# Kernel optimization log

Measured on AMD Instinct MI355X. Metric: run time of the kernel, lower is better.

Reference implementation:

```python
import jax, jax.numpy as jnp
import numpy as np

K = 5
PAD = K // 2
EPS = 1e-12  # F.normalize eps


def setup_inputs() -> dict:
    key = jax.random.key(0)
    k1, k2, k3 = jax.random.split(key, 3)
    b, c, h, w = 8, 1024, 64, 64
    out_ch = 1024
    feature = jax.random.normal(k1, (b, c, h, w), dtype=jnp.float32)
    # Conv2d(1024 + K*K, out_ch, 1) -> weight [out_ch, 1049], bias [out_ch]
    conv_w = jax.random.normal(k2, (out_ch, c + K * K), dtype=jnp.float32) * 0.02
    conv_b = jax.random.normal(k3, (out_ch,), dtype=jnp.float32) * 0.02
    return {"feature": feature, "conv_w": conv_w, "conv_b": conv_b}


def reference(feature, conv_w, conv_b):
    b, c, h, w = feature.shape
    # L2-normalize over channel dim (F.normalize: x / max(||x||, eps))
    norm = jnp.sqrt(jnp.sum(feature * feature, axis=1, keepdims=True))
    fn = feature / jnp.maximum(norm, EPS)
    fp = jnp.pad(fn, ((0, 0), (0, 0), (PAD, PAD), (PAD, PAD)))
    # 25 shifted correlations; order matches torch loop: index = col*K + row
    corr = jnp.stack(
        [jnp.sum(fp[:, :, r:h + r, cc:w + cc] * fn, axis=1)
         for cc in range(K) for r in range(K)],
        axis=1,
    )  # [b, K*K, h, w]
    cat = jnp.concatenate([feature, corr], axis=1)  # [b, c+K*K, h, w]
    y = jnp.einsum('oc,bchw->bohw', conv_w, cat) + conv_b[None, :, None, None]
    return jax.nn.relu(y)
```

## Files before the change

kernel.cpp:

```cpp
#include <hip/hip_runtime.h>
#include <hip/hip_bf16.h>


typedef __attribute__((ext_vector_type(8))) short short8x;
typedef __attribute__((ext_vector_type(4))) float floatx4;

#define B_   8
#define C_   1024
#define HW_  4096
#define KPAD 1088
#define NT   17

__device__ __forceinline__ unsigned short f2bf(float f) {
  unsigned int u = __float_as_uint(f);
  u += 0x7FFFu + ((u >> 16) & 1u);
  return (unsigned short)(u >> 16);
}

__device__ __forceinline__ void async16(const void* g, void* l) {
  __builtin_amdgcn_global_load_lds(
      (__attribute__((address_space(1))) void*)(void*)g,
      (__attribute__((address_space(3))) void*)l, 16, 0, 0);
}

__device__ __forceinline__ short8x rd16(const char* p) {
  return *(const short8x*)p;
}

__global__ __launch_bounds__(512) void scn_aux(
    const float* __restrict__ f, float* __restrict__ corr,
    unsigned short* __restrict__ At, const float* __restrict__ w,
    unsigned short* __restrict__ Wb) {
  __shared__ float lds2[2][64][65];
  const int n = blockIdx.x;
  const int tid = threadIdx.x;

  if (n >= 5120) {
    const int base = (n - 5120) * 4096 + tid * 8;
    const int o = base / KPAD, kk = base - o * KPAD;
    short8x v;
#pragma unroll
    for (int e = 0; e < 8; ++e) {
      const int k = kk + e;
      v[e] = (k < 1049) ? (short)f2bf(w[(size_t)o * 1049 + k]) : (short)0;
    }
    *(short8x*)(Wb + (size_t)o * KPAD + kk) = v;
    return;
  }

  const int g = n / 5, r = n - g * 5;
  if (r == 0) {
    const int x = tid & 63;
    const int y = (g & 7) * 8 + (tid >> 6);
    const int cs = (g >> 3) & 15, b = g >> 7;

    const int xs0 = (x + 2 < 64) ? x + 2 : 63;
    const int xs1 = (x + 1 < 64) ? x + 1 : 63;
    const int xs3 = (x - 1 >= 0) ? x - 1 : 0;
    const int xs4 = (x - 2 >= 0) ? x - 2 : 0;

    const bool ym2 = (y >= 2), ym1 = (y >= 1), yp1 = (y <= 62), yp2 = (y <= 61);

    const float* rp0 = f + ((size_t)b * C_ + cs * 64) * HW_ + y * 64;

    float h[25];
#pragma unroll
    for (int j = 0; j < 25; ++j) h[j] = 0.f;

#pragma unroll 4
    for (int c = 0; c < 64; ++c) {
      const float* rp = rp0 + (size_t)c * HW_;
      const float ctr = rp[x];
      const float vm2 = ym2 ? rp[x - 128] : 0.f;
      const float vm1 = ym1 ? rp[x - 64] : 0.f;
      const float vp1 = yp1 ? rp[x + 64] : 0.f;
      const float vp2 = yp2 ? rp[x + 128] : 0.f;
      const float c0 = __shfl(ctr, xs0, 64);
      const float c1 = __shfl(ctr, xs1, 64);
      const float c3 = __shfl(ctr, xs3, 64);
      const float c4 = __shfl(ctr, xs4, 64);
      const float v[5] = {vm2, vm1, ctr, vp1, vp2};
      const float cc[5] = {c0, c1, ctr, c3, c4};
#pragma unroll
      for (int dxi = 0; dxi < 5; ++dxi)
#pragma unroll
        for (int dyi = 0; dyi < 5; ++dyi)
          h[dxi * 5 + dyi] = fmaf(v[dyi], cc[dxi], h[dxi * 5 + dyi]);
    }

    float* pb = corr + b * HW_ + y * 64;
#pragma unroll
    for (int j = 0; j < 25; ++j) {
      const int dx = (j / 5) - 2;
      const int tgt = x - dx;
      const int wx = (tgt + 64) & 63;
      const float val = ((unsigned)tgt < 64u) ? h[j] : 0.f;
      atomicAdd(pb + (size_t)j * 32768 + wx, val);
    }
  } else {
    const int half = tid >> 8, t256 = tid & 255;
    const int tile = (g * 4 + (r - 1)) * 2 + half;
    const int b = tile >> 10, rem = tile & 1023;
    const int kt = rem >> 6, mt = rem & 63;

    const int m4 = (t256 & 15) << 2, kr0 = t256 >> 4;
    const float* src = f + ((size_t)b * C_ + kt * 64 + kr0) * HW_ + mt * 64 + m4;
#pragma unroll
    for (int i = 0; i < 4; ++i) {
      floatx4 v = *(const floatx4*)(src + (size_t)i * 16 * HW_);
      float* d = &lds2[half][kr0 + i * 16][m4];
      d[0] = v[0]; d[1] = v[1]; d[2] = v[2]; d[3] = v[3];
    }
    __syncthreads();
    unsigned short* dst = At + ((size_t)b * HW_ + mt * 64) * KPAD + kt * 64;
    const int c = t256 & 7, mr = t256 >> 3;
#pragma unroll
    for (int h2 = 0; h2 < 2; ++h2) {
      const int mm = mr + h2 * 32;
      short8x v;
#pragma unroll
      for (int j = 0; j < 8; ++j) v[j] = (short)f2bf(lds2[half][c * 8 + j][mm]);
      *(short8x*)(dst + (size_t)mm * KPAD + c * 8) = v;
    }
  }
}

__global__ __launch_bounds__(256) void scn_reduce2(
    const float* __restrict__ corr, unsigned short* __restrict__ At) {
  __shared__ float linv[8][64];
  const int b = blockIdx.y;
  const int bx = blockIdx.x;
  const int tid = threadIdx.x;
  const int x = tid & 63;
  const int y0 = bx * 4;

  const float* c12 = corr + (size_t)12 * 32768 + b * HW_;
#pragma unroll
  for (int rr = 0; rr < 2; ++rr) {
    const int rsel = (tid >> 6) + rr * 4;
    const int yy = y0 - 2 + rsel;
    const float s = (yy >= 0 && yy < 64) ? c12[yy * 64 + x] : 1.0f;
    linv[rsel][x] = 1.0f / fmaxf(sqrtf(s), 1e-12f);
  }
  __syncthreads();

  const int m = bx * 256 + tid;
  const int i = b * HW_ + m;
  const int yr = tid >> 6;
  const float ic = linv[yr + 2][x];

  unsigned short r[64];
#pragma unroll
  for (int j = 0; j < 25; ++j) {
    const float acc = corr[(size_t)j * 32768 + i];
    const int dy = (j % 5) - 2, dx = (j / 5) - 2;
    const int ny = y0 + yr + dy, nx = x + dx;
    const float in2 = (ny >= 0 && ny < 64 && nx >= 0 && nx < 64)
                          ? linv[yr + 2 + dy][nx] : 0.f;
    r[j] = f2bf(acc * ic * in2);
  }
#pragma unroll
  for (int j = 25; j < 64; ++j) r[j] = 0;
  unsigned short* row = At + ((size_t)b * HW_ + m) * KPAD + 1024;
#pragma unroll
  for (int v = 0; v < 8; ++v) *(short8x*)(row + v * 8) = *(short8x*)(r + v * 8);
}

__global__ __launch_bounds__(512, 2) void scn_gemm(
    const unsigned short* __restrict__ Wb, const unsigned short* __restrict__ At,
    const float* __restrict__ bias, float* __restrict__ out) {
  extern __shared__ char lds[];
  const int tid = threadIdx.x;
  const int l = tid & 63;
  const int wid = tid >> 6;
  const int wm = wid >> 2;
  const int wn = wid & 3;
  const int nb = blockIdx.x, ob = blockIdx.y, b = blockIdx.z;

  const int rr = tid >> 3;
  const int cswz = ((tid & 7) ^ (rr & 7)) << 3;
  const unsigned short* gA = Wb + (size_t)(ob * 256 + rr) * KPAD + cswz;
  const unsigned short* gB = At + ((size_t)b * HW_ + nb * 256 + rr) * KPAD + cswz;
  char* const dBase = (char*)lds + tid * 16;

#define ISSUE_A(bf, kt)                                         \
  do {                                                          \
    const unsigned short* _s = gA + (kt) * 64;                  \
    char* _d = dBase + (bf) * 65536;                            \
    async16(_s, _d);                                            \
    async16(_s + (size_t)64 * KPAD, _d + 8192);                 \
    async16(_s + (size_t)128 * KPAD, _d + 16384);               \
    async16(_s + (size_t)192 * KPAD, _d + 24576);               \
  } while (0)

#define ISSUE_B(bf, kt)                                         \
  do {                                                          \
    const unsigned short* _s = gB + (kt) * 64;                  \
    char* _d = dBase + (bf) * 65536 + 32768;                    \
    async16(_s, _d);                                            \
    async16(_s + (size_t)64 * KPAD, _d + 8192);                 \
    async16(_s + (size_t)128 * KPAD, _d + 16384);               \
    async16(_s + (size_t)192 * KPAD, _d + 24576);               \
  } while (0)

  const int l15 = l & 15, l4g = l >> 4, l7 = l & 7;
  const int aoff0 = l15 * 128 + ((l4g ^ l7) << 4);
  const int aoff1 = l15 * 128 + (((l4g + 4) ^ l7) << 4);
  const char* aB0 = (const char*)lds + wm * 16384;
  const char* bB0 = (const char*)lds + 32768 + (wn >> 1) * 16384 + (wn & 1) * 8192;

  floatx4 acc[8][4];
#pragma unroll
  for (int i = 0; i < 8; ++i)
#pragma unroll
    for (int j = 0; j < 4; ++j) acc[i][j] = (floatx4){0.f, 0.f, 0.f, 0.f};

  ISSUE_A(0, 0); ISSUE_B(0, 0);
  ISSUE_A(1, 1); ISSUE_B(1, 1);
  asm volatile("s_waitcnt vmcnt(8)" ::: "memory");
  __builtin_amdgcn_s_barrier();

  short8x a[4][2], b0[2][2], b1[2][2];

  for (int t = 0; t < NT; ++t) {
    const int bf = t & 1;
    const char* ab = aB0 + bf * 65536;
    const char* bb = bB0 + bf * 65536;
    const int t2 = (t < NT - 2) ? (t + 2) : 0;

#pragma unroll
    for (int i = 0; i < 4; ++i) {
      a[i][0] = rd16(ab + i * 2048 + aoff0);
      a[i][1] = rd16(ab + i * 2048 + aoff1);
    }
#pragma unroll
    for (int j = 0; j < 2; ++j) {
      b0[j][0] = rd16(bb + j * 2048 + aoff0);
      b0[j][1] = rd16(bb + j * 2048 + aoff1);
    }
    __builtin_amdgcn_s_barrier();
    asm volatile("s_waitcnt lgkmcnt(0)" ::: "memory");
    __builtin_amdgcn_sched_barrier(0);
    __builtin_amdgcn_s_setprio(1);
#pragma unroll
    for (int i = 0; i < 4; ++i)
#pragma unroll
      for (int j = 0; j < 2; ++j) {
        acc[i][j] = __builtin_amdgcn_mfma_f32_16x16x32_bf16(a[i][0], b0[j][0], acc[i][j], 0, 0, 0);
        acc[i][j] = __builtin_amdgcn_mfma_f32_16x16x32_bf16(a[i][1], b0[j][1], acc[i][j], 0, 0, 0);
      }
    __builtin_amdgcn_s_setprio(0);
    __builtin_amdgcn_s_barrier();

#pragma unroll
    for (int j = 0; j < 2; ++j) {
      b1[j][0] = rd16(bb + (2 + j) * 2048 + aoff0);
      b1[j][1] = rd16(bb + (2 + j) * 2048 + aoff1);
    }
    __builtin_amdgcn_s_barrier();
    asm volatile("s_waitcnt lgkmcnt(0)" ::: "memory");
    __builtin_amdgcn_sched_barrier(0);
    __builtin_amdgcn_s_setprio(1);
#pragma unroll
    for (int i = 0; i < 4; ++i)
#pragma unroll
      for (int j = 0; j < 2; ++j) {
        acc[i][2 + j] = __builtin_amdgcn_mfma_f32_16x16x32_bf16(a[i][0], b1[j][0], acc[i][2 + j], 0, 0, 0);
        acc[i][2 + j] = __builtin_amdgcn_mfma_f32_16x16x32_bf16(a[i][1], b1[j][1], acc[i][2 + j], 0, 0, 0);
      }
    __builtin_amdgcn_s_setprio(0);
    __builtin_amdgcn_s_barrier();

#pragma unroll
    for (int i = 0; i < 4; ++i) {
      a[i][0] = rd16(ab + (4 + i) * 2048 + aoff0);
      a[i][1] = rd16(ab + (4 + i) * 2048 + aoff1);
    }
    ISSUE_B(bf, t2);
    __builtin_amdgcn_s_barrier();
    asm volatile("s_waitcnt lgkmcnt(0)" ::: "memory");
    __builtin_amdgcn_sched_barrier(0);
    __builtin_amdgcn_s_setprio(1);
#pragma unroll
    for (int i = 0; i < 4; ++i)
#pragma unroll
      for (int j = 0; j < 2; ++j) {
        acc[4 + i][2 + j] = __builtin_amdgcn_mfma_f32_16x16x32_bf16(a[i][0], b1[j][0], acc[4 + i][2 + j], 0, 0, 0);
        acc[4 + i][2 + j] = __builtin_amdgcn_mfma_f32_16x16x32_bf16(a[i][1], b1[j][1], acc[4 + i][2 + j], 0, 0, 0);
      }
    __builtin_amdgcn_s_setprio(0);
    __builtin_amdgcn_s_barrier();

    ISSUE_A(bf, t2);
    __builtin_amdgcn_s_barrier();
    __builtin_amdgcn_s_setprio(1);
#pragma unroll
    for (int i = 0; i < 4; ++i)
#pragma unroll
      for (int j = 0; j < 2; ++j) {
        acc[4 + i][j] = __builtin_amdgcn_mfma_f32_16x16x32_bf16(a[i][0], b0[j][0], acc[4 + i][j], 0, 0, 0);
        acc[4 + i][j] = __builtin_amdgcn_mfma_f32_16x16x32_bf16(a[i][1], b0[j][1], acc[4 + i][j], 0, 0, 0);
      }
    __builtin_amdgcn_s_setprio(0);
    asm volatile("s_waitcnt vmcnt(8)" ::: "memory");
    __builtin_amdgcn_s_barrier();
  }
  asm volatile("s_waitcnt vmcnt(0)" ::: "memory");
#undef ISSUE_A
#undef ISSUE_B

  float* outb = out + (size_t)b * C_ * HW_;
#pragma unroll
  for (int i = 0; i < 8; ++i) {
    const int o0 = ob * 256 + wm * 128 + i * 16 + l4g * 4;
    float bs[4];
#pragma unroll
    for (int r = 0; r < 4; ++r) bs[r] = bias[o0 + r];
#pragma unroll
    for (int j = 0; j < 4; ++j) {
      const int m = nb * 256 + wn * 64 + j * 16 + l15;
#pragma unroll
      for (int r = 0; r < 4; ++r) {
        float v = acc[i][j][r] + bs[r];
        outb[(size_t)(o0 + r) * HW_ + m] = v > 0.f ? v : 0.f;
      }
    }
  }
}

extern "C" void kernel_launch(void* const* d_in, const int* in_sizes, int n_in,
                              void* d_out, int out_size, void* d_ws, size_t ws_size,
                              hipStream_t stream) {
  const float* feature = (const float*)d_in[0];
  const float* conv_w  = (const float*)d_in[1];
  const float* conv_b  = (const float*)d_in[2];
  float* out = (float*)d_out;

  char* ws = (char*)d_ws;
  unsigned short* At = (unsigned short*)(ws);
  float* corr        = (float*)(ws + 71303168);
  unsigned short* Wb = (unsigned short*)(ws + 74579968);

  static int gemm_attr_set = 0;
  if (!gemm_attr_set) {
    hipFuncSetAttribute((const void*)scn_gemm,
                        hipFuncAttributeMaxDynamicSharedMemorySize, 131072);
    gemm_attr_set = 1;
  }

  hipMemsetAsync(corr, 0, 25 * 32768 * sizeof(float), stream);
  scn_aux<<<dim3(5392), 512, 0, stream>>>(feature, corr, At, conv_w, Wb);
  scn_reduce2<<<dim3(16, 8), 256, 0, stream>>>(corr, At);
  scn_gemm<<<dim3(16, 4, 8), 512, 131072, stream>>>(Wb, At, conv_b, out);
}
```

Baseline: 365.7 us.

## Fuse correlation normalization into GEMM prologue and halve correlation channel chunks

The separate normalization kernel is removed. Each GEMM block now computes the inverse norms into LDS and writes the 25 normalized correlation columns of its own At rows before starting the main loop, which saves a launch and a dependency boundary. The correlation pass now splits channels into 32-wide chunks instead of 64, giving more blocks and more parallelism at the cost of twice as many atomic adds. The prologue work is repeated by the four output-channel blocks that share each row tile. Only part of the K padding columns past 1049 is still zeroed; the weight padding there is zero, but leftover workspace contents could still spread NaNs.

```diff
diff --git a/kernel.cpp b/kernel.cpp
--- a/kernel.cpp
+++ b/kernel.cpp
@@ -35,8 +35,8 @@
   const int n = blockIdx.x;
   const int tid = threadIdx.x;
 
-  if (n >= 5120) {
-    const int base = (n - 5120) * 4096 + tid * 8;
+  if (n >= 6144) {
+    const int base = (n - 6144) * 4096 + tid * 8;
     const int o = base / KPAD, kk = base - o * KPAD;
     short8x v;
 #pragma unroll
@@ -48,11 +48,11 @@
     return;
   }
 
-  const int g = n / 5, r = n - g * 5;
+  const int g = n / 3, r = n - g * 3;
   if (r == 0) {
     const int x = tid & 63;
     const int y = (g & 7) * 8 + (tid >> 6);
-    const int cs = (g >> 3) & 15, b = g >> 7;
+    const int cs = (g >> 3) & 31, b = g >> 8;
 
     const int xs0 = (x + 2 < 64) ? x + 2 : 63;
     const int xs1 = (x + 1 < 64) ? x + 1 : 63;
@@ -61,14 +61,14 @@
 
     const bool ym2 = (y >= 2), ym1 = (y >= 1), yp1 = (y <= 62), yp2 = (y <= 61);
 
-    const float* rp0 = f + ((size_t)b * C_ + cs * 64) * HW_ + y * 64;
+    const float* rp0 = f + ((size_t)b * C_ + cs * 32) * HW_ + y * 64;
 
     float h[25];
 #pragma unroll
     for (int j = 0; j < 25; ++j) h[j] = 0.f;
 
 #pragma unroll 4
-    for (int c = 0; c < 64; ++c) {
+    for (int c = 0; c < 32; ++c) {
       const float* rp = rp0 + (size_t)c * HW_;
       const float ctr = rp[x];
       const float vm2 = ym2 ? rp[x - 128] : 0.f;
@@ -99,7 +99,7 @@
     }
   } else {
     const int half = tid >> 8, t256 = tid & 255;
-    const int tile = (g * 4 + (r - 1)) * 2 + half;
+    const int tile = (g * 2 + (r - 1)) * 2 + half;
     const int b = tile >> 10, rem = tile & 1023;
     const int kt = rem >> 6, mt = rem & 63;
 
@@ -125,49 +125,9 @@
   }
 }
 
-__global__ __launch_bounds__(256) void scn_reduce2(
-    const float* __restrict__ corr, unsigned short* __restrict__ At) {
-  __shared__ float linv[8][64];
-  const int b = blockIdx.y;
-  const int bx = blockIdx.x;
-  const int tid = threadIdx.x;
-  const int x = tid & 63;
-  const int y0 = bx * 4;
-
-  const float* c12 = corr + (size_t)12 * 32768 + b * HW_;
-#pragma unroll
-  for (int rr = 0; rr < 2; ++rr) {
-    const int rsel = (tid >> 6) + rr * 4;
-    const int yy = y0 - 2 + rsel;
-    const float s = (yy >= 0 && yy < 64) ? c12[yy * 64 + x] : 1.0f;
-    linv[rsel][x] = 1.0f / fmaxf(sqrtf(s), 1e-12f);
-  }
-  __syncthreads();
-
-  const int m = bx * 256 + tid;
-  const int i = b * HW_ + m;
-  const int yr = tid >> 6;
-  const float ic = linv[yr + 2][x];
-
-  unsigned short r[64];
-#pragma unroll
-  for (int j = 0; j < 25; ++j) {
-    const float acc = corr[(size_t)j * 32768 + i];
-    const int dy = (j % 5) - 2, dx = (j / 5) - 2;
-    const int ny = y0 + yr + dy, nx = x + dx;
-    const float in2 = (ny >= 0 && ny < 64 && nx >= 0 && nx < 64)
-                          ? linv[yr + 2 + dy][nx] : 0.f;
-    r[j] = f2bf(acc * ic * in2);
-  }
-#pragma unroll
-  for (int j = 25; j < 64; ++j) r[j] = 0;
-  unsigned short* row = At + ((size_t)b * HW_ + m) * KPAD + 1024;
-#pragma unroll
-  for (int v = 0; v < 8; ++v) *(short8x*)(row + v * 8) = *(short8x*)(r + v * 8);
-}
-
 __global__ __launch_bounds__(512, 2) void scn_gemm(
-    const unsigned short* __restrict__ Wb, const unsigned short* __restrict__ At,
+    const unsigned short* __restrict__ Wb, const unsigned short* __restrict__ At_c,
+    const float* __restrict__ corr, unsigned short* __restrict__ At,
     const float* __restrict__ bias, float* __restrict__ out) {
   extern __shared__ char lds[];
   const int tid = threadIdx.x;
@@ -176,6 +136,42 @@
   const int wm = wid >> 2;
   const int wn = wid & 3;
   const int nb = blockIdx.x, ob = blockIdx.y, b = blockIdx.z;
+
+  {
+    float* linv = (float*)lds;
+    const int y0 = nb * 4;
+    const float* c12 = corr + (size_t)12 * 32768 + b * HW_;
+    {
+      const int rsel = tid >> 6, xx = tid & 63;
+      const int yy = y0 - 2 + rsel;
+      const float s = (yy >= 0 && yy < 64) ? c12[yy * 64 + xx] : 1.0f;
+      linv[rsel * 64 + xx] = 1.0f / fmaxf(sqrtf(s), 1e-12f);
+    }
+    __syncthreads();
+    if (tid < 256) {
+      const int mm = tid;
+      const int x = mm & 63, yr = mm >> 6;
+      const float ic = linv[(yr + 2) * 64 + x];
+      unsigned short r[64];
+#pragma unroll
+      for (int j = 0; j < 25; ++j) {
+        const float acc = corr[(size_t)j * 32768 + b * HW_ + nb * 256 + mm];
+        const int dy = (j % 5) - 2, dx = (j / 5) - 2;
+        const int ny = y0 + yr + dy, nx = x + dx;
+        const float in2 = (ny >= 0 && ny < 64 && nx >= 0 && nx < 64)
+                              ? linv[(yr + 2 + dy) * 64 + nx] : 0.f;
+        r[j] = f2bf(acc * ic * in2);
+      }
+#pragma unroll
+      for (int j = 25; j < 64; ++j) r[j] = 0;
+      unsigned short* row = At + ((size_t)b * HW_ + nb * 256 + mm) * KPAD + 1024;
+#pragma unroll
+      for (int v = 0; v < 4; ++v)
+        *(short8x*)(row + v * 8) = *(short8x*)(r + v * 8);
+    }
+    asm volatile("s_waitcnt vmcnt(0)" ::: "memory");
+    __syncthreads();
+  }
 
   const int rr = tid >> 3;
   const int cswz = ((tid & 7) ^ (rr & 7)) << 3;
@@ -349,7 +345,6 @@
   }
 
   hipMemsetAsync(corr, 0, 25 * 32768 * sizeof(float), stream);
-  scn_aux<<<dim3(5392), 512, 0, stream>>>(feature, corr, At, conv_w, Wb);
-  scn_reduce2<<<dim3(16, 8), 256, 0, stream>>>(corr, At);
-  scn_gemm<<<dim3(16, 4, 8), 512, 131072, stream>>>(Wb, At, conv_b, out);
-}
+  scn_aux<<<dim3(6416), 512, 0, stream>>>(feature, corr, At, conv_w, Wb);
+  scn_gemm<<<dim3(16, 4, 8), 512, 131072, stream>>>(Wb, At, corr, At, conv_b, out);
+}
```

Result: no change. 373.0 us (+2.0%).
